# Kernel optimization log

Hardware: AMD Instinct MI355X
Metric: run time of the kernel (lower is better)

The kernel has to match this reference:

```python
import jax, jax.numpy as jnp
import numpy as np

B, N, DIM = 4, 4096, 1024
HEADS, DIM_HEAD, M = 16, 64, 128
DIM_INNER = HEADS * DIM_HEAD
SCALE = DIM_HEAD ** -0.5


def setup_inputs() -> dict:
    key = jax.random.key(0)
    ks = jax.random.split(key, 7)
    x = jax.random.normal(ks[0], (B, N, DIM), dtype=jnp.float32)
    mask = jax.random.bernoulli(ks[1], 0.9, (B, N))  # bool [b, n]
    W_qkv = jax.random.normal(ks[2], (DIM, 3 * DIM_INNER), dtype=jnp.float32) * (DIM ** -0.5)
    agent_tokens = jax.random.normal(ks[3], (HEADS, M, DIM_HEAD), dtype=jnp.float32) * 0.02
    W_qa = jax.random.normal(ks[4], (HEADS, HEADS), dtype=jnp.float32) * (HEADS ** -0.5)
    W_ak = jax.random.normal(ks[5], (HEADS, HEADS), dtype=jnp.float32) * (HEADS ** -0.5)
    W_out = jax.random.normal(ks[6], (DIM_INNER, DIM), dtype=jnp.float32) * (DIM_INNER ** -0.5)
    return {"x": x, "mask": mask, "W_qkv": W_qkv, "agent_tokens": agent_tokens,
            "W_qa": W_qa, "W_ak": W_ak, "W_out": W_out}


def reference(x, mask, W_qkv, agent_tokens, W_qa, W_ak, W_out):
    b, n, _ = x.shape
    h, m, d = agent_tokens.shape
    # qkv projection -> [3, b, h, n, d]  (layout matches 'b n (qkv h d)')
    qkv = (x @ W_qkv).reshape(b, n, 3, h, d).transpose(2, 0, 3, 1, 4)
    q, k, v = qkv[0], qkv[1], qkv[2]
    a = agent_tokens * SCALE  # [h, m, d]
    # stage 1: query-agent similarities [b, h, n, m]
    qa_sim = jnp.einsum('bhid,hjd->bhij', q, a)
    # stage 2: agent-key similarities [b, h, m, n]
    ak_sim = jnp.einsum('hid,bhjd->bhij', a, k)
    max_neg = -jnp.finfo(ak_sim.dtype).max
    ak_sim = jnp.where(mask[:, None, None, :], ak_sim, max_neg)
    qa_attn = jax.nn.softmax(qa_sim, axis=-1)
    ak_attn = jax.nn.softmax(ak_sim, axis=-1)
    # talking heads: 1x1 conv over head dim == head-mixing matmul
    qa_attn = jnp.einsum('gh,bhij->bgij', W_qa, qa_attn)
    ak_attn = jnp.einsum('gh,bhij->bgij', W_ak, ak_attn)
    agent_out = jnp.einsum('bhmn,bhnd->bhmd', ak_attn, v)    # [b, h, m, d]
    out = jnp.einsum('bhnm,bhmd->bhnd', qa_attn, agent_out)  # [b, h, n, d]
    out = jnp.where(mask[:, None, :, None], out, 0.0)
    out = out.transpose(0, 2, 1, 3).reshape(b, n, h * d)
    return out @ W_out
```

## Files before the change

### kernel.cpp

```cpp
#include <hip/hip_runtime.h>
#include <stdint.h>

#define DEVI __device__ __forceinline__

typedef __bf16 bf16x8 __attribute__((ext_vector_type(8)));
typedef float  f32x4  __attribute__((ext_vector_type(4)));
typedef unsigned int u32x2 __attribute__((ext_vector_type(2)));


DEVI unsigned short f2bf(float f) {
  union { float f; unsigned int u; } c; c.f = f;
  return (unsigned short)((c.u + 0x7fffu + ((c.u >> 16) & 1u)) >> 16);
}
DEVI float bf2f(unsigned short s) {
  union { unsigned int u; float f; } c; c.u = ((unsigned int)s) << 16;
  return c.f;
}
DEVI u32x2 pack4(float a, float b, float c, float d) {
  u32x2 r;
  r.x = (unsigned)f2bf(a) | ((unsigned)f2bf(b) << 16);
  r.y = (unsigned)f2bf(c) | ((unsigned)f2bf(d) << 16);
  return r;
}
DEVI bf16x8 ldg8(const unsigned short* p) { return *(const bf16x8*)p; }

DEVI void g2l16(const void* g, void* l) {
  __builtin_amdgcn_global_load_lds(
      (const __attribute__((address_space(1))) unsigned int*)g,
      (__attribute__((address_space(3))) unsigned int*)l, 16, 0, 0);
}

#define MFMA16(acc, a, b) acc = __builtin_amdgcn_mfma_f32_16x16x32_bf16((a), (b), (acc), 0, 0, 0)

__global__ __launch_bounds__(256) void k_prep(
    const float* __restrict__ x, const float* __restrict__ Wqkv,
    const float* __restrict__ ag, const float* __restrict__ Wout,
    unsigned short* __restrict__ Xb, unsigned short* __restrict__ WqkvT,
    unsigned short* __restrict__ Ab, unsigned short* __restrict__ WoT,
    float* __restrict__ rowsum)
{
  __shared__ float ldsT[32][33];
  const int tid = threadIdx.x;
  int bx = blockIdx.x;
  if (bx < 16384) {
    size_t i4 = ((size_t)bx * 256 + tid) * 4;
    f32x4 v = *(const f32x4*)&x[i4];
    *(u32x2*)&Xb[i4] = pack4(v[0], v[1], v[2], v[3]);
    return;
  }
  bx -= 16384;
  if (bx < 3072) {
    int jt = bx % 96, kt = bx / 96;
    int r32 = tid >> 3, c4 = (tid & 7) * 4;
    f32x4 v = *(const f32x4*)&Wqkv[(size_t)(kt * 32 + r32) * 3072 + jt * 32 + c4];
#pragma unroll
    for (int i = 0; i < 4; i++) ldsT[r32][c4 + i] = v[i];
    __syncthreads();
    float o0 = ldsT[c4 + 0][r32], o1 = ldsT[c4 + 1][r32];
    float o2 = ldsT[c4 + 2][r32], o3 = ldsT[c4 + 3][r32];
    *(u32x2*)&WqkvT[(size_t)(jt * 32 + r32) * 1024 + kt * 32 + c4] = pack4(o0, o1, o2, o3);
    return;
  }
  bx -= 3072;
  if (bx < 128) {
    size_t i4 = ((size_t)bx * 256 + tid) * 4;
    f32x4 v = *(const f32x4*)&ag[i4];
    *(u32x2*)&Ab[i4] = pack4(v[0] * 0.125f, v[1] * 0.125f, v[2] * 0.125f, v[3] * 0.125f);
    return;
  }
  bx -= 128;
  if (bx < 1024) {
    int ct = bx % 32, dt = bx / 32;
    int r32 = tid >> 3, c4 = (tid & 7) * 4;
    f32x4 v = *(const f32x4*)&Wout[(size_t)(dt * 32 + r32) * 1024 + ct * 32 + c4];
#pragma unroll
    for (int i = 0; i < 4; i++) ldsT[r32][c4 + i] = v[i];
    __syncthreads();
    float o0 = ldsT[c4 + 0][r32], o1 = ldsT[c4 + 1][r32];
    float o2 = ldsT[c4 + 2][r32], o3 = ldsT[c4 + 3][r32];
    *(u32x2*)&WoT[(size_t)(ct * 32 + r32) * 1024 + dt * 32 + c4] = pack4(o0, o1, o2, o3);
    return;
  }
  bx -= 1024;
  {
    const f32x4 z = {0.f, 0.f, 0.f, 0.f};
    *(f32x4*)&rowsum[((size_t)bx * 256 + tid) * 4] = z;
  }
}

__global__ __launch_bounds__(256, 2) void k_gemm_qkv(
    const unsigned short* __restrict__ A, const unsigned short* __restrict__ Bt,
    unsigned short* __restrict__ Q, unsigned short* __restrict__ Kd,
    unsigned short* __restrict__ Vt)
{
  __shared__ __align__(16) unsigned short lA[4096];
  __shared__ __align__(16) unsigned short lB[4096];
  const int tid = threadIdx.x, lane = tid & 63, w = tid >> 6;
  const int q = lane >> 4, r = lane & 15, wr = w >> 1, wc = w & 1;
  const int row0 = blockIdx.x * 128, col0 = blockIdx.y * 128;
  const bool qk = blockIdx.y < 16;
  const int c1 = w, c2 = w + 4;
  const int sr1 = c1 * 16 + (lane >> 2), sr2 = c2 * 16 + (lane >> 2);
  const int sk = 8 * (lane & 3);
  const unsigned short* gA1 = A + (size_t)(row0 + sr1) * 1024 + sk;
  const unsigned short* gA2 = A + (size_t)(row0 + sr2) * 1024 + sk;
  const unsigned short* gB1 = Bt + (size_t)(col0 + sr1) * 1024 + sk;
  const unsigned short* gB2 = Bt + (size_t)(col0 + sr2) * 1024 + sk;
  const unsigned short* sA = qk ? lB : lA;
  const unsigned short* sB = qk ? lA : lB;
  f32x4 acc[4][4];
  const f32x4 z = {0.f, 0.f, 0.f, 0.f};
#pragma unroll
  for (int i = 0; i < 4; i++)
#pragma unroll
    for (int j = 0; j < 4; j++) acc[i][j] = z;

  for (int k0 = 0; k0 < 1024; k0 += 32) {
    g2l16(gA1 + k0, &lA[c1 * 512]);
    g2l16(gA2 + k0, &lA[c2 * 512]);
    g2l16(gB1 + k0, &lB[c1 * 512]);
    g2l16(gB2 + k0, &lB[c2 * 512]);
    __syncthreads();
    bf16x8 af[4], bv[4];
#pragma unroll
    for (int rt = 0; rt < 4; rt++) af[rt] = *(const bf16x8*)&sA[(64 * wr + 16 * rt + r) * 32 + q * 8];
#pragma unroll
    for (int ct = 0; ct < 4; ct++) bv[ct] = *(const bf16x8*)&sB[(64 * wc + 16 * ct + r) * 32 + q * 8];
#pragma unroll
    for (int rt = 0; rt < 4; rt++)
#pragma unroll
      for (int ct = 0; ct < 4; ct++) MFMA16(acc[rt][ct], af[rt], bv[ct]);
    __syncthreads();
  }
  const int b = row0 >> 12;
  if (qk) {
    unsigned short* dst = (blockIdx.y < 8) ? Q : Kd;
    const int hbase = ((col0 & 1023) >> 6) + wr;
#pragma unroll
    for (int rt = 0; rt < 4; rt++)
#pragma unroll
      for (int ct = 0; ct < 4; ct++) {
        int d0 = 16 * rt + 4 * q;
        int n = (row0 & 4095) + 64 * wc + 16 * ct + r;
        u32x2 pk = pack4(acc[rt][ct][0], acc[rt][ct][1], acc[rt][ct][2], acc[rt][ct][3]);
        *(u32x2*)&dst[(((size_t)(b * 16 + hbase)) * 4096 + n) * 64 + d0] = pk;
      }
  } else {
#pragma unroll
    for (int rt = 0; rt < 4; rt++)
#pragma unroll
      for (int ct = 0; ct < 4; ct++) {
        int j = (col0 - 2048) + 64 * wc + 16 * ct + r;
        int h = j >> 6, d = j & 63;
        int nb = (row0 & 4095) + 64 * wr + 16 * rt + 4 * q;
        u32x2 pk = pack4(acc[rt][ct][0], acc[rt][ct][1], acc[rt][ct][2], acc[rt][ct][3]);
        *(u32x2*)&Vt[(((size_t)(b * 16 + h)) * 64 + d) * 4096 + nb] = pk;
      }
  }
}

__global__ __launch_bounds__(256, 2) void k_qk(
    const unsigned short* __restrict__ Q, const unsigned short* __restrict__ Kd,
    const unsigned short* __restrict__ Ab, const int* __restrict__ mask,
    unsigned short* __restrict__ QA, unsigned short* __restrict__ E,
    float* __restrict__ rowsum)
{
  const int tid = threadIdx.x, lane = tid & 63, w = tid >> 6;
  const int q = lane >> 4, r = lane & 15, wr = w >> 1, wc = w & 1;
  const int nt = blockIdx.x, h = blockIdx.y, b = blockIdx.z;
  const unsigned short* Qb = Q + (((size_t)(b * 16 + h)) * 4096 + nt * 128) * 64;
  const unsigned short* Kb = Kd + (((size_t)(b * 16 + h)) * 4096 + nt * 128) * 64;
  const unsigned short* Ah = Ab + (size_t)h * 8192;
  __shared__ float rs[2][128];
  const f32x4 z = {0.f, 0.f, 0.f, 0.f};

  {
    f32x4 acc[4][4];
#pragma unroll
    for (int i = 0; i < 4; i++)
#pragma unroll
      for (int j = 0; j < 4; j++) acc[i][j] = z;
#pragma unroll
    for (int ks = 0; ks < 2; ks++) {
      bf16x8 af[4], bv[4];
#pragma unroll
      for (int rt = 0; rt < 4; rt++) af[rt] = ldg8(Ah + (size_t)(64 * wr + 16 * rt + r) * 64 + ks * 32 + q * 8);
#pragma unroll
      for (int ct = 0; ct < 4; ct++) bv[ct] = ldg8(Qb + (size_t)(64 * wc + 16 * ct + r) * 64 + ks * 32 + q * 8);
#pragma unroll
      for (int rt = 0; rt < 4; rt++)
#pragma unroll
        for (int ct = 0; ct < 4; ct++) MFMA16(acc[rt][ct], af[rt], bv[ct]);
    }
    float cs[4];
#pragma unroll
    for (int ct = 0; ct < 4; ct++) {
      float s = 0.f;
#pragma unroll
      for (int rt = 0; rt < 4; rt++)
#pragma unroll
        for (int reg = 0; reg < 4; reg++) {
          float e = __expf(acc[rt][ct][reg]);
          acc[rt][ct][reg] = e; s += e;
        }
      s += __shfl_xor(s, 16); s += __shfl_xor(s, 32);
      cs[ct] = s;
    }
    if (q == 0) {
#pragma unroll
      for (int ct = 0; ct < 4; ct++) rs[wr][64 * wc + 16 * ct + r] = cs[ct];
    }
    __syncthreads();
#pragma unroll
    for (int ct = 0; ct < 4; ct++) {
      int nl = 64 * wc + 16 * ct + r;
      float inv = 1.0f / (rs[0][nl] + rs[1][nl]);
      int n = nt * 128 + nl;
      size_t base = (((size_t)(b * 16 + h)) * 4096 + n) * 128;
#pragma unroll
      for (int rt = 0; rt < 4; rt++) {
        int m0 = 64 * wr + 16 * rt + 4 * q;
        u32x2 pk = pack4(acc[rt][ct][0] * inv, acc[rt][ct][1] * inv,
                         acc[rt][ct][2] * inv, acc[rt][ct][3] * inv);
        *(u32x2*)&QA[base + m0] = pk;
      }
    }
  }
  __syncthreads();

  {
    f32x4 acc[4][4];
#pragma unroll
    for (int i = 0; i < 4; i++)
#pragma unroll
      for (int j = 0; j < 4; j++) acc[i][j] = z;
#pragma unroll
    for (int ks = 0; ks < 2; ks++) {
      bf16x8 af[4], bv[4];
#pragma unroll
      for (int rt = 0; rt < 4; rt++) af[rt] = ldg8(Kb + (size_t)(64 * wr + 16 * rt + r) * 64 + ks * 32 + q * 8);
#pragma unroll
      for (int ct = 0; ct < 4; ct++) bv[ct] = ldg8(Ah + (size_t)(64 * wc + 16 * ct + r) * 64 + ks * 32 + q * 8);
#pragma unroll
      for (int rt = 0; rt < 4; rt++)
#pragma unroll
        for (int ct = 0; ct < 4; ct++) MFMA16(acc[rt][ct], af[rt], bv[ct]);
    }
    float cs[4] = {0.f, 0.f, 0.f, 0.f};
#pragma unroll
    for (int rt = 0; rt < 4; rt++) {
      const int4 mkv = *(const int4*)&mask[b * 4096 + nt * 128 + 64 * wr + 16 * rt + 4 * q];
      int mka[4] = {mkv.x, mkv.y, mkv.z, mkv.w};
#pragma unroll
      for (int ct = 0; ct < 4; ct++) {
#pragma unroll
        for (int reg = 0; reg < 4; reg++) {
          float e = mka[reg] ? __expf(acc[rt][ct][reg]) : 0.0f;
          acc[rt][ct][reg] = e; cs[ct] += e;
        }
      }
    }
#pragma unroll
    for (int ct = 0; ct < 4; ct++) {
      float s = cs[ct];
      s += __shfl_xor(s, 16); s += __shfl_xor(s, 32);
      cs[ct] = s;
    }
    if (q == 0) {
#pragma unroll
      for (int ct = 0; ct < 4; ct++) rs[wr][64 * wc + 16 * ct + r] = cs[ct];
    }
#pragma unroll
    for (int ct = 0; ct < 4; ct++) {
      int m = 64 * wc + 16 * ct + r;
      size_t base = (((size_t)(b * 16 + h)) * 128 + m) * 4096;
#pragma unroll
      for (int rt = 0; rt < 4; rt++) {
        int n0 = nt * 128 + 64 * wr + 16 * rt + 4 * q;
        u32x2 pk = pack4(acc[rt][ct][0], acc[rt][ct][1], acc[rt][ct][2], acc[rt][ct][3]);
        *(u32x2*)&E[base + n0] = pk;
      }
    }
    __syncthreads();
    if (tid < 128) atomicAdd(&rowsum[(b * 16 + h) * 128 + tid], rs[0][tid] + rs[1][tid]);
  }
}

__global__ __launch_bounds__(256) void k_mix(
    const unsigned short* __restrict__ E, const float* __restrict__ rowsum,
    const float* __restrict__ Wak, unsigned short* __restrict__ MIX)
{
  const int tid = threadIdx.x;
  const int m = blockIdx.y, b = blockIdx.z;
  __shared__ float wv[256];
  __shared__ float inv[16];
  wv[tid] = Wak[tid];
  if (tid < 16) inv[tid] = 1.0f / rowsum[(b * 16 + tid) * 128 + m];
  __syncthreads();
  const int n0 = (blockIdx.x * 256 + tid) * 4;
  float p[16][4];
#pragma unroll
  for (int h = 0; h < 16; h++) {
    u32x2 v = *(const u32x2*)&E[(((size_t)(b * 16 + h)) * 128 + m) * 4096 + n0];
    float iv = inv[h];
    p[h][0] = bf2f((unsigned short)(v.x & 0xffff)) * iv;
    p[h][1] = bf2f((unsigned short)(v.x >> 16)) * iv;
    p[h][2] = bf2f((unsigned short)(v.y & 0xffff)) * iv;
    p[h][3] = bf2f((unsigned short)(v.y >> 16)) * iv;
  }
#pragma unroll
  for (int g = 0; g < 16; g++) {
    float s0 = 0.f, s1 = 0.f, s2 = 0.f, s3 = 0.f;
#pragma unroll
    for (int h = 0; h < 16; h++) {
      float wgh = wv[g * 16 + h];
      s0 += wgh * p[h][0]; s1 += wgh * p[h][1]; s2 += wgh * p[h][2]; s3 += wgh * p[h][3];
    }
    *(u32x2*)&MIX[(((size_t)(b * 16 + g)) * 128 + m) * 4096 + n0] = pack4(s0, s1, s2, s3);
  }
}

__global__ __launch_bounds__(256) void k_ao(
    const unsigned short* __restrict__ MIX, const unsigned short* __restrict__ Vt,
    float* __restrict__ P)
{
  const int tid = threadIdx.x, lane = tid & 63, w4 = tid >> 6;
  const int q = lane >> 4, r = lane & 15;
  const int kc = blockIdx.x, g = blockIdx.y, b = blockIdx.z;
  const unsigned short* Abase = MIX + ((size_t)(b * 16 + g)) * 128 * 4096;
  const unsigned short* Bbase = Vt + ((size_t)(b * 16 + g)) * 64 * 4096;
  f32x4 acc[2][4];
  const f32x4 z = {0.f, 0.f, 0.f, 0.f};
#pragma unroll
  for (int i = 0; i < 2; i++)
#pragma unroll
    for (int j = 0; j < 4; j++) acc[i][j] = z;
  for (int n = kc * 512; n < kc * 512 + 512; n += 32) {
    bf16x8 af[2], bv[4];
#pragma unroll
    for (int rt = 0; rt < 2; rt++) af[rt] = ldg8(Abase + (size_t)(32 * w4 + 16 * rt + r) * 4096 + n + q * 8);
#pragma unroll
    for (int ct = 0; ct < 4; ct++) bv[ct] = ldg8(Bbase + (size_t)(16 * ct + r) * 4096 + n + q * 8);
#pragma unroll
    for (int rt = 0; rt < 2; rt++)
#pragma unroll
      for (int ct = 0; ct < 4; ct++) MFMA16(acc[rt][ct], af[rt], bv[ct]);
  }
  float* Pp = P + (size_t)kc * 524288 + ((size_t)(b * 16 + g)) * 8192;
#pragma unroll
  for (int rt = 0; rt < 2; rt++)
#pragma unroll
    for (int ct = 0; ct < 4; ct++) {
      int m0 = 32 * w4 + 16 * rt + 4 * q, d = 16 * ct + r;
      *(f32x4*)&Pp[(size_t)d * 128 + m0] = acc[rt][ct];
    }
}

__global__ __launch_bounds__(256) void k_aored(
    const float* __restrict__ P, float* __restrict__ AOt)
{
  size_t i = ((size_t)blockIdx.x * 256 + threadIdx.x) * 4;
  f32x4 s = *(const f32x4*)&P[i];
#pragma unroll
  for (int kc = 1; kc < 8; kc++) {
    f32x4 v = *(const f32x4*)&P[(size_t)kc * 524288 + i];
    s[0] += v[0]; s[1] += v[1]; s[2] += v[2]; s[3] += v[3];
  }
  *(f32x4*)&AOt[i] = s;
}

__global__ __launch_bounds__(256) void k_mixqa(
    const unsigned short* __restrict__ QA, const float* __restrict__ Wqa,
    unsigned short* __restrict__ QAmix)
{
  const int tid = threadIdx.x;
  const int b = blockIdx.y;
  __shared__ float wv[256];
  wv[tid] = Wqa[tid];
  __syncthreads();
  const size_t i0 = ((size_t)blockIdx.x * 256 + tid) * 4;
  float p[16][4];
#pragma unroll
  for (int h = 0; h < 16; h++) {
    u32x2 v = *(const u32x2*)&QA[((size_t)(b * 16 + h)) * 524288 + i0];
    p[h][0] = bf2f((unsigned short)(v.x & 0xffff));
    p[h][1] = bf2f((unsigned short)(v.x >> 16));
    p[h][2] = bf2f((unsigned short)(v.y & 0xffff));
    p[h][3] = bf2f((unsigned short)(v.y >> 16));
  }
#pragma unroll
  for (int g = 0; g < 16; g++) {
    float s0 = 0.f, s1 = 0.f, s2 = 0.f, s3 = 0.f;
#pragma unroll
    for (int h = 0; h < 16; h++) {
      float wgh = wv[g * 16 + h];
      s0 += wgh * p[h][0]; s1 += wgh * p[h][1]; s2 += wgh * p[h][2]; s3 += wgh * p[h][3];
    }
    *(u32x2*)&QAmix[((size_t)(b * 16 + g)) * 524288 + i0] = pack4(s0, s1, s2, s3);
  }
}

__global__ __launch_bounds__(256) void k_o1(
    const unsigned short* __restrict__ QAmix, const float* __restrict__ AOt,
    unsigned short* __restrict__ out1)
{
  const int tid = threadIdx.x, lane = tid & 63, w4 = tid >> 6;
  const int q = lane >> 4, r = lane & 15;
  const int nt = blockIdx.x, g = blockIdx.y, b = blockIdx.z;
  const unsigned short* Bbase = QAmix + (((size_t)(b * 16 + g)) * 4096 + nt * 128) * 128;
  const float* Abase = AOt + ((size_t)(b * 16 + g)) * 8192;
  f32x4 acc[4][2];
  const f32x4 z = {0.f, 0.f, 0.f, 0.f};
#pragma unroll
  for (int i = 0; i < 4; i++)
#pragma unroll
    for (int j = 0; j < 2; j++) acc[i][j] = z;
#pragma unroll
  for (int ks = 0; ks < 4; ks++) {
    bf16x8 af[4], bv[2];
#pragma unroll
    for (int rt = 0; rt < 4; rt++) {
      const float* p = Abase + (size_t)(16 * rt + r) * 128 + ks * 32 + q * 8;
      f32x4 f0 = *(const f32x4*)p;
      f32x4 f1 = *(const f32x4*)(p + 4);
      bf16x8 t;
#pragma unroll
      for (int jj = 0; jj < 4; jj++) { t[jj] = (__bf16)f0[jj]; t[4 + jj] = (__bf16)f1[jj]; }
      af[rt] = t;
    }
#pragma unroll
    for (int ct = 0; ct < 2; ct++)
      bv[ct] = ldg8(Bbase + (size_t)(32 * w4 + 16 * ct + r) * 128 + ks * 32 + q * 8);
#pragma unroll
    for (int rt = 0; rt < 4; rt++)
#pragma unroll
      for (int ct = 0; ct < 2; ct++) MFMA16(acc[rt][ct], af[rt], bv[ct]);
  }
#pragma unroll
  for (int ct = 0; ct < 2; ct++) {
    int n = nt * 128 + 32 * w4 + 16 * ct + r;
    size_t base = ((size_t)b * 4096 + n) * 1024 + g * 64;
#pragma unroll
    for (int rt = 0; rt < 4; rt++) {
      int d0 = 16 * rt + 4 * q;
      u32x2 pk = pack4(acc[rt][ct][0], acc[rt][ct][1], acc[rt][ct][2], acc[rt][ct][3]);
      *(u32x2*)&out1[base + d0] = pk;
    }
  }
}

__global__ __launch_bounds__(256, 2) void k_fin2(
    const unsigned short* __restrict__ A, const unsigned short* __restrict__ Bt,
    const int* __restrict__ mask, float* __restrict__ out)
{
  __shared__ __align__(16) unsigned short lA[4096];
  __shared__ __align__(16) unsigned short lB[4096];
  const int tid = threadIdx.x, lane = tid & 63, w = tid >> 6;
  const int q = lane >> 4, r = lane & 15, wr = w >> 1, wc = w & 1;
  const int row0 = blockIdx.x * 128, col0 = blockIdx.y * 128;
  const int c1 = w, c2 = w + 4;
  const int sr1 = c1 * 16 + (lane >> 2), sr2 = c2 * 16 + (lane >> 2);
  const int sk = 8 * (lane & 3);
  const unsigned short* gA1 = A + (size_t)(row0 + sr1) * 1024 + sk;
  const unsigned short* gA2 = A + (size_t)(row0 + sr2) * 1024 + sk;
  const unsigned short* gB1 = Bt + (size_t)(col0 + sr1) * 1024 + sk;
  const unsigned short* gB2 = Bt + (size_t)(col0 + sr2) * 1024 + sk;
  f32x4 acc[4][4];
  const f32x4 z = {0.f, 0.f, 0.f, 0.f};
#pragma unroll
  for (int i = 0; i < 4; i++)
#pragma unroll
    for (int j = 0; j < 4; j++) acc[i][j] = z;
  for (int k0 = 0; k0 < 1024; k0 += 32) {
    g2l16(gA1 + k0, &lA[c1 * 512]);
    g2l16(gA2 + k0, &lA[c2 * 512]);
    g2l16(gB1 + k0, &lB[c1 * 512]);
    g2l16(gB2 + k0, &lB[c2 * 512]);
    __syncthreads();
    bf16x8 af[4], bv[4];
#pragma unroll
    for (int rt = 0; rt < 4; rt++) af[rt] = *(const bf16x8*)&lA[(64 * wr + 16 * rt + r) * 32 + q * 8];
#pragma unroll
    for (int ct = 0; ct < 4; ct++) bv[ct] = *(const bf16x8*)&lB[(64 * wc + 16 * ct + r) * 32 + q * 8];
#pragma unroll
    for (int rt = 0; rt < 4; rt++)
#pragma unroll
      for (int ct = 0; ct < 4; ct++) MFMA16(acc[rt][ct], af[rt], bv[ct]);
    __syncthreads();
  }
#pragma unroll
  for (int rt = 0; rt < 4; rt++)
#pragma unroll
    for (int reg = 0; reg < 4; reg++) {
      int row = row0 + 64 * wr + 16 * rt + 4 * q + reg;
      int mv = mask[row];
#pragma unroll
      for (int ct = 0; ct < 4; ct++) {
        int c = col0 + 64 * wc + 16 * ct + r;
        out[(size_t)row * 1024 + c] = mv ? acc[rt][ct][reg] : 0.0f;
      }
    }
}

extern "C" void kernel_launch(void* const* d_in, const int* in_sizes, int n_in,
                              void* d_out, int out_size, void* d_ws, size_t ws_size,
                              hipStream_t stream) {
  const float* x    = (const float*)d_in[0];
  const int*   mask = (const int*)d_in[1];
  const float* Wqkv = (const float*)d_in[2];
  const float* ag   = (const float*)d_in[3];
  const float* Wqa  = (const float*)d_in[4];
  const float* Wak  = (const float*)d_in[5];
  const float* Wout = (const float*)d_in[6];
  float* out = (float*)d_out;
  char* ws = (char*)d_ws;

  unsigned short* QA    = (unsigned short*)(ws + 0);
  unsigned short* QQ    = (unsigned short*)(ws + 67108864);
  unsigned short* KK    = (unsigned short*)(ws + 67108864 + 33554432);
  unsigned short* MIX   = QQ;
  unsigned short* out1  = QQ;
  unsigned short* VT    = (unsigned short*)(ws + 134217728);
  unsigned short* Xb    = (unsigned short*)(ws + 167772160);
  unsigned short* WqkvT = (unsigned short*)(ws + 167772160 + 33554432);
  unsigned short* E     = Xb;
  float*          Ppart = (float*)Xb;
  unsigned short* QAmix = Xb;
  char* sm = ws + 234881024;
  unsigned short* Ab  = (unsigned short*)(sm);
  unsigned short* WoT = (unsigned short*)(sm + 262144);
  float* rowsum = (float*)(sm + 262144 + 2097152);
  float* AOt    = (float*)(sm + 262144 + 2097152 + 32768);

  k_prep<<<20616, 256, 0, stream>>>(x, Wqkv, ag, Wout, Xb, WqkvT, Ab, WoT, rowsum);
  k_gemm_qkv<<<dim3(128, 24), 256, 0, stream>>>(Xb, WqkvT, QQ, KK, VT);
  k_qk<<<dim3(32, 16, 4), 256, 0, stream>>>(QQ, KK, Ab, mask, QA, E, rowsum);
  k_mix<<<dim3(4, 128, 4), 256, 0, stream>>>(E, rowsum, Wak, MIX);
  k_ao<<<dim3(8, 16, 4), 256, 0, stream>>>(MIX, VT, Ppart);
  k_aored<<<512, 256, 0, stream>>>(Ppart, AOt);
  k_mixqa<<<dim3(512, 4), 256, 0, stream>>>(QA, Wqa, QAmix);
  k_o1<<<dim3(32, 16, 4), 256, 0, stream>>>(QAmix, AOt, out1);
  k_fin2<<<dim3(128, 8), 256, 0, stream>>>(out1, WoT, mask, out);
}
```

Measured before the change: 502.1 us.

## Pipeline QKV and output GEMMs with 256x256 tiles and a 4-stage async LDS ring

Replaces the two 128x128 single-buffered GEMM kernels with a shared 256x256-tile core using 512 threads. The core keeps a four-slot LDS ring filled by direct global-to-LDS loads issued three steps ahead, with explicit vmcnt waits, raw barriers, an XOR swizzle to cut LDS bank conflicts, and setprio around the MFMA bursts. This targets exposed global-load latency and the low reuse of the earlier tiles. In exchange it uses 128KB of LDS per block and many more accumulator registers, and the output grid shrinks to 768 and 256 blocks, which may leave CUs idle on the smaller GEMM.

```diff
diff --git a/kernel.cpp b/kernel.cpp
--- a/kernel.cpp
+++ b/kernel.cpp
@@ -31,6 +31,11 @@
 }
 
 #define MFMA16(acc, a, b) acc = __builtin_amdgcn_mfma_f32_16x16x32_bf16((a), (b), (acc), 0, 0, 0)
+
+#define VMCNT8() asm volatile("s_waitcnt vmcnt(8)" ::: "memory")
+#define VMCNT4() asm volatile("s_waitcnt vmcnt(4)" ::: "memory")
+#define VMCNT0() asm volatile("s_waitcnt vmcnt(0)" ::: "memory")
+#define SBAR() do { asm volatile("" ::: "memory"); __builtin_amdgcn_s_barrier(); asm volatile("" ::: "memory"); } while (0)
 
 __global__ __launch_bounds__(256) void k_prep(
     const float* __restrict__ x, const float* __restrict__ Wqkv,
@@ -88,73 +93,126 @@
   }
 }
 
-__global__ __launch_bounds__(256, 2) void k_gemm_qkv(
+DEVI void gemm_core_256(const unsigned short* __restrict__ A,
+                        const unsigned short* __restrict__ Bt,
+                        int row0, int col0, int swap,
+                        unsigned short (*lds)[16384], f32x4 acc[8][4])
+{
+  const int tid = threadIdx.x, lane = tid & 63, w = tid >> 6;
+  const int q = lane >> 4, r = lane & 15;
+  const int wm = w >> 2, wn = w & 3;
+  const int loff = r * 32 + ((q ^ ((r >> 1) & 3)) << 3);
+  const int wslot = w * 512;
+  const int scol = ((tid & 3) ^ ((tid >> 3) & 3)) << 3;
+  const int srow = tid >> 2;
+  const unsigned short* gA0 = A + (size_t)(row0 + srow) * 1024 + scol;
+  const unsigned short* gA1 = gA0 + (size_t)128 * 1024;
+  const unsigned short* gB0 = Bt + (size_t)(col0 + srow) * 1024 + scol;
+  const unsigned short* gB1 = gB0 + (size_t)128 * 1024;
+  const int aoff = (swap ? 8192 : 0) + wm * 4096;
+  const int boff = (swap ? 0 : 8192) + wn * 2048;
+
+  const f32x4 z = {0.f, 0.f, 0.f, 0.f};
+#pragma unroll
+  for (int i = 0; i < 8; i++)
+#pragma unroll
+    for (int j = 0; j < 4; j++) acc[i][j] = z;
+
+#pragma unroll
+  for (int pt = 0; pt < 3; ++pt) {
+    unsigned short* lr = &lds[pt][0] + wslot;
+    g2l16(gA0 + pt * 32, lr);
+    g2l16(gA1 + pt * 32, lr + 4096);
+    g2l16(gB0 + pt * 32, lr + 8192);
+    g2l16(gB1 + pt * 32, lr + 12288);
+  }
+  VMCNT8();
+  SBAR();
+
+  for (int t = 0; t < 32; ++t) {
+    const unsigned short* rp = &lds[t & 3][0];
+    const unsigned short* pA = rp + aoff + loff;
+    const unsigned short* pB = rp + boff + loff;
+    bf16x8 af[4], bv[4];
+#pragma unroll
+    for (int rt = 0; rt < 4; rt++) af[rt] = *(const bf16x8*)(pA + rt * 512);
+#pragma unroll
+    for (int ct = 0; ct < 4; ct++) bv[ct] = *(const bf16x8*)(pB + ct * 512);
+    if (t < 29) {
+      unsigned short* lr = &lds[(t + 3) & 3][0] + wslot;
+      size_t ko = (size_t)(t + 3) * 32;
+      g2l16(gA0 + ko, lr);
+      g2l16(gA1 + ko, lr + 4096);
+    }
+    SBAR();
+    __builtin_amdgcn_s_setprio(1);
+#pragma unroll
+    for (int rt = 0; rt < 4; rt++)
+#pragma unroll
+      for (int ct = 0; ct < 4; ct++) MFMA16(acc[rt][ct], af[rt], bv[ct]);
+    __builtin_amdgcn_s_setprio(0);
+    SBAR();
+#pragma unroll
+    for (int rt = 0; rt < 4; rt++) af[rt] = *(const bf16x8*)(pA + (rt + 4) * 512);
+    if (t < 29) {
+      unsigned short* lr = &lds[(t + 3) & 3][0] + wslot;
+      size_t ko = (size_t)(t + 3) * 32;
+      g2l16(gB0 + ko, lr + 8192);
+      g2l16(gB1 + ko, lr + 12288);
+    }
+    if (t < 29)      { VMCNT8(); }
+    else if (t == 29) { VMCNT4(); }
+    else if (t == 30) { VMCNT0(); }
+    SBAR();
+    __builtin_amdgcn_s_setprio(1);
+#pragma unroll
+    for (int rt = 0; rt < 4; rt++)
+#pragma unroll
+      for (int ct = 0; ct < 4; ct++) MFMA16(acc[rt + 4][ct], af[rt], bv[ct]);
+    __builtin_amdgcn_s_setprio(0);
+    SBAR();
+  }
+}
+
+__global__ __launch_bounds__(512, 2) void k_gemm_qkv(
     const unsigned short* __restrict__ A, const unsigned short* __restrict__ Bt,
     unsigned short* __restrict__ Q, unsigned short* __restrict__ Kd,
     unsigned short* __restrict__ Vt)
 {
-  __shared__ __align__(16) unsigned short lA[4096];
-  __shared__ __align__(16) unsigned short lB[4096];
+  __shared__ __align__(16) unsigned short lds[4][16384];
   const int tid = threadIdx.x, lane = tid & 63, w = tid >> 6;
-  const int q = lane >> 4, r = lane & 15, wr = w >> 1, wc = w & 1;
-  const int row0 = blockIdx.x * 128, col0 = blockIdx.y * 128;
-  const bool qk = blockIdx.y < 16;
-  const int c1 = w, c2 = w + 4;
-  const int sr1 = c1 * 16 + (lane >> 2), sr2 = c2 * 16 + (lane >> 2);
-  const int sk = 8 * (lane & 3);
-  const unsigned short* gA1 = A + (size_t)(row0 + sr1) * 1024 + sk;
-  const unsigned short* gA2 = A + (size_t)(row0 + sr2) * 1024 + sk;
-  const unsigned short* gB1 = Bt + (size_t)(col0 + sr1) * 1024 + sk;
-  const unsigned short* gB2 = Bt + (size_t)(col0 + sr2) * 1024 + sk;
-  const unsigned short* sA = qk ? lB : lA;
-  const unsigned short* sB = qk ? lA : lB;
-  f32x4 acc[4][4];
-  const f32x4 z = {0.f, 0.f, 0.f, 0.f};
-#pragma unroll
-  for (int i = 0; i < 4; i++)
-#pragma unroll
-    for (int j = 0; j < 4; j++) acc[i][j] = z;
-
-  for (int k0 = 0; k0 < 1024; k0 += 32) {
-    g2l16(gA1 + k0, &lA[c1 * 512]);
-    g2l16(gA2 + k0, &lA[c2 * 512]);
-    g2l16(gB1 + k0, &lB[c1 * 512]);
-    g2l16(gB2 + k0, &lB[c2 * 512]);
-    __syncthreads();
-    bf16x8 af[4], bv[4];
-#pragma unroll
-    for (int rt = 0; rt < 4; rt++) af[rt] = *(const bf16x8*)&sA[(64 * wr + 16 * rt + r) * 32 + q * 8];
-#pragma unroll
-    for (int ct = 0; ct < 4; ct++) bv[ct] = *(const bf16x8*)&sB[(64 * wc + 16 * ct + r) * 32 + q * 8];
-#pragma unroll
-    for (int rt = 0; rt < 4; rt++)
-#pragma unroll
-      for (int ct = 0; ct < 4; ct++) MFMA16(acc[rt][ct], af[rt], bv[ct]);
-    __syncthreads();
-  }
-  const int b = row0 >> 12;
+  const int q = lane >> 4, r = lane & 15, wm = w >> 2, wn = w & 3;
+  const int row0 = blockIdx.x * 256, col0 = blockIdx.y * 256;
+  const bool qk = blockIdx.y < 8;
+
+  f32x4 acc[8][4];
+  gemm_core_256(A, Bt, row0, col0, qk ? 1 : 0, lds, acc);
+
+  const int b = row0 >> 12, row0b = row0 & 4095;
   if (qk) {
-    unsigned short* dst = (blockIdx.y < 8) ? Q : Kd;
-    const int hbase = ((col0 & 1023) >> 6) + wr;
-#pragma unroll
-    for (int rt = 0; rt < 4; rt++)
+    unsigned short* dst = (col0 < 1024) ? Q : Kd;
+    const int jb = (col0 & 1023) + wm * 128;
+#pragma unroll
+    for (int rt = 0; rt < 8; rt++)
 #pragma unroll
       for (int ct = 0; ct < 4; ct++) {
-        int d0 = 16 * rt + 4 * q;
-        int n = (row0 & 4095) + 64 * wc + 16 * ct + r;
+        int j = jb + rt * 16 + 4 * q;
+        int h = j >> 6, d0 = j & 63;
+        int n = row0b + wn * 64 + ct * 16 + r;
         u32x2 pk = pack4(acc[rt][ct][0], acc[rt][ct][1], acc[rt][ct][2], acc[rt][ct][3]);
-        *(u32x2*)&dst[(((size_t)(b * 16 + hbase)) * 4096 + n) * 64 + d0] = pk;
+        *(u32x2*)&dst[(((size_t)(b * 16 + h)) * 4096 + n) * 64 + d0] = pk;
       }
   } else {
-#pragma unroll
-    for (int rt = 0; rt < 4; rt++)
+    const int jb = (col0 - 2048) + wn * 64;
+#pragma unroll
+    for (int rt = 0; rt < 8; rt++)
 #pragma unroll
       for (int ct = 0; ct < 4; ct++) {
-        int j = (col0 - 2048) + 64 * wc + 16 * ct + r;
+        int j = jb + ct * 16 + r;
         int h = j >> 6, d = j & 63;
-        int nb = (row0 & 4095) + 64 * wr + 16 * rt + 4 * q;
+        int n = row0b + wm * 128 + rt * 16 + 4 * q;
         u32x2 pk = pack4(acc[rt][ct][0], acc[rt][ct][1], acc[rt][ct][2], acc[rt][ct][3]);
-        *(u32x2*)&Vt[(((size_t)(b * 16 + h)) * 64 + d) * 4096 + nb] = pk;
+        *(u32x2*)&Vt[(((size_t)(b * 16 + h)) * 64 + d) * 4096 + n] = pk;
       }
   }
 }
@@ -449,57 +507,32 @@
   }
 }
 
-__global__ __launch_bounds__(256, 2) void k_fin2(
+__global__ __launch_bounds__(512, 2) void k_fin2(
     const unsigned short* __restrict__ A, const unsigned short* __restrict__ Bt,
     const int* __restrict__ mask, float* __restrict__ out)
 {
-  __shared__ __align__(16) unsigned short lA[4096];
-  __shared__ __align__(16) unsigned short lB[4096];
+  __shared__ __align__(16) unsigned short lds[4][16384];
   const int tid = threadIdx.x, lane = tid & 63, w = tid >> 6;
-  const int q = lane >> 4, r = lane & 15, wr = w >> 1, wc = w & 1;
-  const int row0 = blockIdx.x * 128, col0 = blockIdx.y * 128;
-  const int c1 = w, c2 = w + 4;
-  const int sr1 = c1 * 16 + (lane >> 2), sr2 = c2 * 16 + (lane >> 2);
-  const int sk = 8 * (lane & 3);
-  const unsigned short* gA1 = A + (size_t)(row0 + sr1) * 1024 + sk;
-  const unsigned short* gA2 = A + (size_t)(row0 + sr2) * 1024 + sk;
-  const unsigned short* gB1 = Bt + (size_t)(col0 + sr1) * 1024 + sk;
-  const unsigned short* gB2 = Bt + (size_t)(col0 + sr2) * 1024 + sk;
-  f32x4 acc[4][4];
-  const f32x4 z = {0.f, 0.f, 0.f, 0.f};
-#pragma unroll
-  for (int i = 0; i < 4; i++)
-#pragma unroll
-    for (int j = 0; j < 4; j++) acc[i][j] = z;
-  for (int k0 = 0; k0 < 1024; k0 += 32) {
-    g2l16(gA1 + k0, &lA[c1 * 512]);
-    g2l16(gA2 + k0, &lA[c2 * 512]);
-    g2l16(gB1 + k0, &lB[c1 * 512]);
-    g2l16(gB2 + k0, &lB[c2 * 512]);
-    __syncthreads();
-    bf16x8 af[4], bv[4];
-#pragma unroll
-    for (int rt = 0; rt < 4; rt++) af[rt] = *(const bf16x8*)&lA[(64 * wr + 16 * rt + r) * 32 + q * 8];
-#pragma unroll
-    for (int ct = 0; ct < 4; ct++) bv[ct] = *(const bf16x8*)&lB[(64 * wc + 16 * ct + r) * 32 + q * 8];
-#pragma unroll
-    for (int rt = 0; rt < 4; rt++)
-#pragma unroll
-      for (int ct = 0; ct < 4; ct++) MFMA16(acc[rt][ct], af[rt], bv[ct]);
-    __syncthreads();
-  }
-#pragma unroll
-  for (int rt = 0; rt < 4; rt++)
+  const int q = lane >> 4, r = lane & 15, wm = w >> 2, wn = w & 3;
+  const int row0 = blockIdx.x * 256, col0 = blockIdx.y * 256;
+
+  f32x4 acc[8][4];
+  gemm_core_256(A, Bt, row0, col0, 0, lds, acc);
+
+#pragma unroll
+  for (int rt = 0; rt < 8; rt++) {
+    const int4 mkv = *(const int4*)&mask[row0 + wm * 128 + rt * 16 + 4 * q];
+    int mka[4] = {mkv.x, mkv.y, mkv.z, mkv.w};
 #pragma unroll
     for (int reg = 0; reg < 4; reg++) {
-      int row = row0 + 64 * wr + 16 * rt + 4 * q + reg;
-      int mv = mask[row];
+      int row = row0 + wm * 128 + rt * 16 + 4 * q + reg;
 #pragma unroll
       for (int ct = 0; ct < 4; ct++) {
-        int c = col0 + 64 * wc + 16 * ct + r;
-        out[(size_t)row * 1024 + c] = mv ? acc[rt][ct][reg] : 0.0f;
+        int c = col0 + wn * 64 + ct * 16 + r;
+        out[(size_t)row * 1024 + c] = mka[reg] ? acc[rt][ct][reg] : 0.0f;
       }
     }
+  }
 }
 
 extern "C" void kernel_launch(void* const* d_in, const int* in_sizes, int n_in,
@@ -533,12 +566,12 @@
   float* AOt    = (float*)(sm + 262144 + 2097152 + 32768);
 
   k_prep<<<20616, 256, 0, stream>>>(x, Wqkv, ag, Wout, Xb, WqkvT, Ab, WoT, rowsum);
-  k_gemm_qkv<<<dim3(128, 24), 256, 0, stream>>>(Xb, WqkvT, QQ, KK, VT);
+  k_gemm_qkv<<<dim3(64, 12), 512, 0, stream>>>(Xb, WqkvT, QQ, KK, VT);
   k_qk<<<dim3(32, 16, 4), 256, 0, stream>>>(QQ, KK, Ab, mask, QA, E, rowsum);
   k_mix<<<dim3(4, 128, 4), 256, 0, stream>>>(E, rowsum, Wak, MIX);
   k_ao<<<dim3(8, 16, 4), 256, 0, stream>>>(MIX, VT, Ppart);
   k_aored<<<512, 256, 0, stream>>>(Ppart, AOt);
   k_mixqa<<<dim3(512, 4), 256, 0, stream>>>(QA, Wqa, QAmix);
   k_o1<<<dim3(32, 16, 4), 256, 0, stream>>>(QAmix, AOt, out1);
-  k_fin2<<<dim3(128, 8), 256, 0, stream>>>(out1, WoT, mask, out);
-}
+  k_fin2<<<dim3(64, 4), 512, 0, stream>>>(out1, WoT, mask, out);
+}
```

After: 480.9 us. 4.2% less time.
